# Kernel tuning notes

Hardware: AMD Instinct MI355X
Metric: run time of the kernel (lower is better)

Reference implementation:

```python
import jax, jax.numpy as jnp
import numpy as np

N, E, F_IN, H = 50000, 800000, 500, 96

def setup_inputs() -> dict:
    key = jax.random.key(0)
    ks = jax.random.split(key, 10)
    x = jax.random.normal(ks[0], (N, F_IN), dtype=jnp.float32)
    src = jax.random.randint(ks[1], (E,), 0, N, dtype=jnp.int32)
    dst = jax.random.randint(ks[2], (E,), 0, N, dtype=jnp.int32)
    perm = jax.random.permutation(ks[3], N).astype(jnp.int32)
    W1 = jax.random.normal(ks[4], (F_IN, H), dtype=jnp.float32) / np.sqrt(F_IN)
    b1 = jnp.zeros((H,), jnp.float32)
    a1 = jnp.full((H,), 0.25, jnp.float32)  # PReLU init
    W2 = jax.random.normal(ks[5], (H, H), dtype=jnp.float32) / np.sqrt(H)
    b2 = jnp.zeros((H,), jnp.float32)
    a2 = jnp.full((H,), 0.25, jnp.float32)
    Wm = jax.random.normal(ks[6], (H, H), dtype=jnp.float32) / np.sqrt(H)
    bm = jnp.zeros((H,), jnp.float32)
    return {"x": x, "src": src, "dst": dst, "perm": perm,
            "W1": W1, "b1": b1, "a1": a1, "W2": W2, "b2": b2, "a2": a2,
            "Wm": Wm, "bm": bm}

def reference(x, src, dst, perm, W1, b1, a1, W2, b2, a2, Wm, bm):
    n = x.shape[0]
    ones = jnp.ones_like(src, dtype=x.dtype)
    deg_out = jnp.clip(jax.ops.segment_sum(ones, src, num_segments=n), 1.0)
    deg_in = jnp.clip(jax.ops.segment_sum(ones, dst, num_segments=n), 1.0)
    norm_out = (deg_out ** -0.5)[:, None]  # [N,1]
    norm_in = (deg_in ** -0.5)[:, None]

    def gconv(h, W, b, a):
        # DGL GraphConv, norm='both': D_out^-1/2 -> W -> A -> D_in^-1/2 -> +b -> PReLU
        h = (h * norm_out) @ W                                  # [N,H]
        agg = jax.ops.segment_sum(h[src], dst, num_segments=n)  # SpMM via gather/scatter
        h = agg * norm_in + b
        return jnp.where(h >= 0, h, a * h)                      # PReLU

    def encode(feat):
        h = gconv(feat, W1, b1, a1)
        return gconv(h, W2, b2, a2)

    z1 = encode(x)
    z2 = encode(x[perm])  # corrupted view: permuted node features
    z1 = z1 @ Wm + bm
    z2 = z2 @ Wm + bm
    return jnp.concatenate([z1.sum(1), z2.sum(1)], axis=0)  # [2N]
```

## Files before the change

kernel.cpp:

```cpp
#include <hip/hip_runtime.h>

#define H96 96

typedef __attribute__((ext_vector_type(8))) short bf16x8_t;
typedef __attribute__((ext_vector_type(4))) float f32x4_t;
typedef __attribute__((ext_vector_type(8))) _Float16 half8_t;

__global__ void deg_kernel(const int* __restrict__ src, const int* __restrict__ dst,
                           int* __restrict__ dout, int* __restrict__ din, int E) {
    int e = blockIdx.x * blockDim.x + threadIdx.x;
    if (e < E) {
        atomicAdd(dout + src[e], 1);
        atomicAdd(din + dst[e], 1);
    }
}

__global__ void norm_kernel(const int* __restrict__ dO, const int* __restrict__ dI,
                            float* __restrict__ no, float* __restrict__ ni, int N) {
    int i = blockIdx.x * blockDim.x + threadIdx.x;
    if (i < N) {
        no[i] = rsqrtf(fmaxf((float)dO[i], 1.0f));
        ni[i] = rsqrtf(fmaxf((float)dI[i], 1.0f));
    }
}

__global__ void scanA_kernel(const int* __restrict__ in, int* __restrict__ pre,
                             int* __restrict__ bsums, int n) {
    __shared__ int s[256];
    int i = blockIdx.x * 256 + threadIdx.x;
    int v = (i < n) ? in[i] : 0;
    s[threadIdx.x] = v;
    __syncthreads();
    for (int off = 1; off < 256; off <<= 1) {
        int t = (threadIdx.x >= off) ? s[threadIdx.x - off] : 0;
        __syncthreads();
        s[threadIdx.x] += t;
        __syncthreads();
    }
    if (i < n) pre[i] = s[threadIdx.x] - v;
    if (threadIdx.x == 255) bsums[blockIdx.x] = s[255];
}

__global__ void scanB_kernel(int* __restrict__ bsums, int nb) {
    __shared__ int s[256];
    int v = (threadIdx.x < nb) ? bsums[threadIdx.x] : 0;
    s[threadIdx.x] = v;
    __syncthreads();
    for (int off = 1; off < 256; off <<= 1) {
        int t = (threadIdx.x >= off) ? s[threadIdx.x - off] : 0;
        __syncthreads();
        s[threadIdx.x] += t;
        __syncthreads();
    }
    if (threadIdx.x < nb) bsums[threadIdx.x] = s[threadIdx.x] - v;
}

__global__ void rowfin_kernel(const int* __restrict__ pre, const int* __restrict__ bsums,
                              int* __restrict__ row_start, int* __restrict__ cursor,
                              int N, int E) {
    int i = blockIdx.x * 256 + threadIdx.x;
    if (i < N) {
        int v = pre[i] + bsums[blockIdx.x];
        row_start[i] = v;
        cursor[i] = v;
    }
    if (i == 0) row_start[N] = E;
}

__global__ void scatter_kernel(const int* __restrict__ src, const int* __restrict__ dst,
                               const int* __restrict__ perm, const float* __restrict__ norm_out,
                               int* __restrict__ cursor, int4* __restrict__ edge4, int E) {
    int e = blockIdx.x * 256 + threadIdx.x;
    if (e < E) {
        int d = dst[e];
        int s = src[e];
        int p = atomicAdd(cursor + d, 1);
        edge4[p] = make_int4(s, perm[s], __float_as_int(norm_out[s]), 0);
    }
}

__global__ void histblk_kernel(const int* __restrict__ deg, int* __restrict__ hb,
                               int N, int nb) {
    __shared__ int h[256];
    h[threadIdx.x] = 0;
    __syncthreads();
    int i = blockIdx.x * 256 + threadIdx.x;
    if (i < N) atomicAdd(&h[min(deg[i], 255)], 1);
    __syncthreads();
    hb[threadIdx.x * nb + blockIdx.x] = h[threadIdx.x];
}

__global__ void place2_kernel(const int* __restrict__ deg, const int* __restrict__ hpre,
                              const int* __restrict__ bsums, int* __restrict__ order,
                              int N, int nb) {
    __shared__ int cur[256];
    int idx = threadIdx.x * nb + blockIdx.x;
    cur[threadIdx.x] = hpre[idx] + bsums[idx >> 8];
    __syncthreads();
    int i = blockIdx.x * 256 + threadIdx.x;
    if (i < N) {
        int b = min(deg[i], 255);
        int p = atomicAdd(&cur[b], 1);
        order[p] = i;
    }
}

__device__ __forceinline__ void f2bf2(float v, unsigned short& h, unsigned short& l) {
    unsigned int b = __float_as_uint(v);
    unsigned short hh = (unsigned short)((b + 0x7FFFu + ((b >> 16) & 1u)) >> 16);
    float fh = __uint_as_float(((unsigned int)hh) << 16);
    float r = v - fh;
    unsigned int rb = __float_as_uint(r);
    unsigned short ll = (unsigned short)((rb + 0x7FFFu + ((rb >> 16) & 1u)) >> 16);
    h = hh; l = ll;
}

__global__ void weights_prep(const float* __restrict__ W1, const float* __restrict__ W2,
                             const float* __restrict__ Wm, const float* __restrict__ bm,
                             unsigned short* __restrict__ w1h, unsigned short* __restrict__ w1l,
                             unsigned short* __restrict__ w2h, unsigned short* __restrict__ w2l,
                             float* __restrict__ wsum, float* __restrict__ bsum,
                             int F, int KP1) {
    int idx = blockIdx.x * 256 + threadIdx.x;
    int z1 = 96 * KP1, z2 = z1 + 96 * 96;
    if (idx < z1) {
        int n = idx / KP1, k = idx - n * KP1;
        float v = (k < F) ? W1[(size_t)k * 96 + n] : 0.f;
        unsigned short h, l;
        f2bf2(v, h, l);
        w1h[idx] = h; w1l[idx] = l;
    } else if (idx < z2) {
        int t = idx - z1;
        int n = t / 96, k = t - n * 96;
        float v = W2[(size_t)k * 96 + n];
        unsigned short h, l;
        f2bf2(v, h, l);
        w2h[t] = h; w2l[t] = l;
    } else if (idx < z2 + 96) {
        int c = idx - z2;
        float s = 0.f;
        for (int j = 0; j < 96; j++) s += Wm[c * 96 + j];
        wsum[c] = s;
    } else if (idx == z2 + 96) {
        float s = 0.f;
        for (int j = 0; j < 96; j++) s += bm[j];
        bsum[0] = s;
    }
}

#define GBM 64
#define GBK 32
#define ASTR2 40
__global__ __launch_bounds__(256) void gemm_mfma(const void* __restrict__ Av,
                                                 const unsigned short* __restrict__ Bth,
                                                 const unsigned short* __restrict__ Btl,
                                                 _Float16* __restrict__ C16,
                                                 int M, int K, int KP, int a_half) {
    __shared__ unsigned short As_hi[GBM * ASTR2];
    __shared__ unsigned short As_lo[GBM * ASTR2];
    __shared__ unsigned short Bs_hi[96 * ASTR2];
    __shared__ unsigned short Bs_lo[96 * ASTR2];
    int tid = threadIdx.x;
    int row0 = blockIdx.x * GBM;
    int wid = tid >> 6, lane = tid & 63;
    int q = lane >> 4, mn = lane & 15;
    f32x4_t acc[6] = {};
    int nk = (K + GBK - 1) / GBK;

    const float* A32 = (const float*)Av;
    const _Float16* A16 = (const _Float16*)Av;

    for (int t = 0; t < nk; t++) {
        int k0 = t * GBK;
        if (a_half) {
            int r = tid >> 2, kq = tid & 3;
            int gr = row0 + r, gk = k0 + kq * 8;
            uint4 raw = (gr < M) ? *(const uint4*)(A16 + (size_t)gr * K + gk)
                                 : make_uint4(0, 0, 0, 0);
            const _Float16* hp = (const _Float16*)&raw;
            unsigned short hs[8], ls[8];
#pragma unroll
            for (int c = 0; c < 8; c++) f2bf2((float)hp[c], hs[c], ls[c]);
            uint4 hv, lv;
            hv.x = hs[0] | ((unsigned)hs[1] << 16); hv.y = hs[2] | ((unsigned)hs[3] << 16);
            hv.z = hs[4] | ((unsigned)hs[5] << 16); hv.w = hs[6] | ((unsigned)hs[7] << 16);
            lv.x = ls[0] | ((unsigned)ls[1] << 16); lv.y = ls[2] | ((unsigned)ls[3] << 16);
            lv.z = ls[4] | ((unsigned)ls[5] << 16); lv.w = ls[6] | ((unsigned)ls[7] << 16);
            *(uint4*)&As_hi[r * ASTR2 + kq * 8] = hv;
            *(uint4*)&As_lo[r * ASTR2 + kq * 8] = lv;
        } else {
#pragma unroll
            for (int i = 0; i < 2; i++) {
                int idx = tid + i * 256;
                int r = idx >> 3, kq = idx & 7;
                int gr = row0 + r, gk = k0 + kq * 4;
                float4 v = make_float4(0.f, 0.f, 0.f, 0.f);
                if (gr < M) {
                    if (gk + 4 <= K) {
                        v = *(const float4*)(A32 + (size_t)gr * K + gk);
                    } else {
                        float tv[4] = {0.f, 0.f, 0.f, 0.f};
                        for (int c = 0; c < 4; c++)
                            if (gk + c < K) tv[c] = A32[(size_t)gr * K + gk + c];
                        v = make_float4(tv[0], tv[1], tv[2], tv[3]);
                    }
                }
                unsigned short h0, l0, h1, l1, h2, l2, h3, l3;
                f2bf2(v.x, h0, l0); f2bf2(v.y, h1, l1);
                f2bf2(v.z, h2, l2); f2bf2(v.w, h3, l3);
                uint2 hv = make_uint2((unsigned)h0 | ((unsigned)h1 << 16),
                                      (unsigned)h2 | ((unsigned)h3 << 16));
                uint2 lv = make_uint2((unsigned)l0 | ((unsigned)l1 << 16),
                                      (unsigned)l2 | ((unsigned)l3 << 16));
                *(uint2*)&As_hi[r * ASTR2 + kq * 4] = hv;
                *(uint2*)&As_lo[r * ASTR2 + kq * 4] = lv;
            }
        }
#pragma unroll
        for (int i = 0; i < 2; i++) {
            int idx = tid + i * 256;
            if (idx < 384) {
                int n = idx >> 2, kc = idx & 3;
                uint4 hv = *(const uint4*)(Bth + (size_t)n * KP + k0 + kc * 8);
                uint4 lv = *(const uint4*)(Btl + (size_t)n * KP + k0 + kc * 8);
                *(uint4*)&Bs_hi[n * ASTR2 + kc * 8] = hv;
                *(uint4*)&Bs_lo[n * ASTR2 + kc * 8] = lv;
            }
        }
        __syncthreads();

        int wr = wid * 16 + mn;
        bf16x8_t ah = *(const bf16x8_t*)&As_hi[wr * ASTR2 + q * 8];
        bf16x8_t al = *(const bf16x8_t*)&As_lo[wr * ASTR2 + q * 8];
#pragma unroll
        for (int ct = 0; ct < 6; ct++) {
            int n = ct * 16 + mn;
            bf16x8_t bh = *(const bf16x8_t*)&Bs_hi[n * ASTR2 + q * 8];
            bf16x8_t bl = *(const bf16x8_t*)&Bs_lo[n * ASTR2 + q * 8];
            acc[ct] = __builtin_amdgcn_mfma_f32_16x16x32_bf16(ah, bh, acc[ct], 0, 0, 0);
            acc[ct] = __builtin_amdgcn_mfma_f32_16x16x32_bf16(ah, bl, acc[ct], 0, 0, 0);
            acc[ct] = __builtin_amdgcn_mfma_f32_16x16x32_bf16(al, bh, acc[ct], 0, 0, 0);
        }
        __syncthreads();
    }

#pragma unroll
    for (int reg = 0; reg < 4; reg++) {
        int gr = row0 + wid * 16 + q * 4 + reg;
        if (gr < M) {
#pragma unroll
            for (int ct = 0; ct < 6; ct++)
                C16[(size_t)gr * H96 + ct * 16 + mn] = (_Float16)acc[ct][reg];
        }
    }
}

__device__ __forceinline__ void fmah8(float4& a, float4& b, float s, half8_t v) {
    a.x = fmaf(s, (float)v[0], a.x); a.y = fmaf(s, (float)v[1], a.y);
    a.z = fmaf(s, (float)v[2], a.z); a.w = fmaf(s, (float)v[3], a.w);
    b.x = fmaf(s, (float)v[4], b.x); b.y = fmaf(s, (float)v[5], b.y);
    b.z = fmaf(s, (float)v[6], b.z); b.w = fmaf(s, (float)v[7], b.w);
}

__device__ __forceinline__ float4 prelu4(float4 acc, float ni, float4 b, float4 a) {
    float4 h;
    h.x = fmaf(acc.x, ni, b.x); h.x = (h.x >= 0.f) ? h.x : a.x * h.x;
    h.y = fmaf(acc.y, ni, b.y); h.y = (h.y >= 0.f) ? h.y : a.y * h.y;
    h.z = fmaf(acc.z, ni, b.z); h.z = (h.z >= 0.f) ? h.z : a.z * h.z;
    h.w = fmaf(acc.w, ni, b.w); h.w = (h.w >= 0.f) ? h.w : a.w * h.w;
    return h;
}

__global__ __launch_bounds__(384) void spmm1_dual(
        const half8_t* __restrict__ yh, const int* __restrict__ row_start,
        const int4* __restrict__ edge4, const int* __restrict__ order,
        const float* __restrict__ norm_out, const float* __restrict__ norm_in,
        const float* __restrict__ b1, const float* __restrict__ a1,
        half8_t* __restrict__ h1, half8_t* __restrict__ h2, int N) {
    int g = blockIdx.x * 32 + threadIdx.y;
    if (g >= N) return;
    int d = order[g];
    int tx = threadIdx.x;
    int beg = row_start[d], end = row_start[d + 1];
    const half8_t* yt = yh + tx;
    float4 a1a = {0,0,0,0}, a1b = {0,0,0,0}, a2a = {0,0,0,0}, a2b = {0,0,0,0};
    int j = beg;
    for (; j + 8 <= end; j += 8) {
        int4 e[8];
#pragma unroll
        for (int q = 0; q < 8; q++) e[q] = edge4[j + q];
        half8_t u[8], w[8];
#pragma unroll
        for (int q = 0; q < 8; q++) u[q] = yt[(size_t)e[q].x * 12];
#pragma unroll
        for (int q = 0; q < 8; q++) w[q] = yt[(size_t)e[q].y * 12];
#pragma unroll
        for (int q = 0; q < 8; q++) {
            float n = __int_as_float(e[q].z);
            fmah8(a1a, a1b, n, u[q]);
            fmah8(a2a, a2b, n, w[q]);
        }
    }
    for (; j < end; j++) {
        int4 e = edge4[j];
        float n = __int_as_float(e.z);
        fmah8(a1a, a1b, n, yt[(size_t)e.x * 12]);
        fmah8(a2a, a2b, n, yt[(size_t)e.y * 12]);
    }
    float ni = norm_in[d], no = norm_out[d];
    float4 bb0 = ((const float4*)b1)[tx * 2], bb1 = ((const float4*)b1)[tx * 2 + 1];
    float4 aa0 = ((const float4*)a1)[tx * 2], aa1 = ((const float4*)a1)[tx * 2 + 1];
    float4 r1a = prelu4(a1a, ni, bb0, aa0), r1b = prelu4(a1b, ni, bb1, aa1);
    float4 r2a = prelu4(a2a, ni, bb0, aa0), r2b = prelu4(a2b, ni, bb1, aa1);
    half8_t o1, o2;
    o1[0] = (_Float16)(r1a.x * no); o1[1] = (_Float16)(r1a.y * no);
    o1[2] = (_Float16)(r1a.z * no); o1[3] = (_Float16)(r1a.w * no);
    o1[4] = (_Float16)(r1b.x * no); o1[5] = (_Float16)(r1b.y * no);
    o1[6] = (_Float16)(r1b.z * no); o1[7] = (_Float16)(r1b.w * no);
    o2[0] = (_Float16)(r2a.x * no); o2[1] = (_Float16)(r2a.y * no);
    o2[2] = (_Float16)(r2a.z * no); o2[3] = (_Float16)(r2a.w * no);
    o2[4] = (_Float16)(r2b.x * no); o2[5] = (_Float16)(r2b.y * no);
    o2[6] = (_Float16)(r2b.z * no); o2[7] = (_Float16)(r2b.w * no);
    h1[(size_t)d * 12 + tx] = o1;
    h2[(size_t)d * 12 + tx] = o2;
}

__global__ __launch_bounds__(384) void spmm2_dual(
        const half8_t* __restrict__ th,
        const int* __restrict__ row_start, const int4* __restrict__ edge4,
        const int* __restrict__ order, const float* __restrict__ norm_in,
        const float* __restrict__ b2, const float* __restrict__ a2,
        const float* __restrict__ wsum, const float* __restrict__ bsum,
        float* __restrict__ outp, int N) {
    int g = blockIdx.x * 32 + threadIdx.y;
    int tx = threadIdx.x;
    int ty = threadIdx.y;
    bool valid = (g < N);
    int d = valid ? order[g] : 0;
    int beg = 0, end = 0;
    if (valid) { beg = row_start[d]; end = row_start[d + 1]; }
    const half8_t* t1 = th + tx;
    const half8_t* t2 = th + (size_t)N * 12 + tx;
    float4 a1a = {0,0,0,0}, a1b = {0,0,0,0}, a2a = {0,0,0,0}, a2b = {0,0,0,0};
    int j = beg;
    for (; j + 8 <= end; j += 8) {
        int s[8];
#pragma unroll
        for (int q = 0; q < 8; q++) s[q] = edge4[j + q].x;
        half8_t u[8], w[8];
#pragma unroll
        for (int q = 0; q < 8; q++) u[q] = t1[(size_t)s[q] * 12];
#pragma unroll
        for (int q = 0; q < 8; q++) w[q] = t2[(size_t)s[q] * 12];
#pragma unroll
        for (int q = 0; q < 8; q++) {
            fmah8(a1a, a1b, 1.f, u[q]);
            fmah8(a2a, a2b, 1.f, w[q]);
        }
    }
    for (; j < end; j++) {
        int s = edge4[j].x;
        fmah8(a1a, a1b, 1.f, t1[(size_t)s * 12]);
        fmah8(a2a, a2b, 1.f, t2[(size_t)s * 12]);
    }
    float ni = valid ? norm_in[d] : 0.f;
    float4 bb0 = ((const float4*)b2)[tx * 2], bb1 = ((const float4*)b2)[tx * 2 + 1];
    float4 aa0 = ((const float4*)a2)[tx * 2], aa1 = ((const float4*)a2)[tx * 2 + 1];
    float4 wv0 = ((const float4*)wsum)[tx * 2], wv1 = ((const float4*)wsum)[tx * 2 + 1];
    float4 r1a = prelu4(a1a, ni, bb0, aa0), r1b = prelu4(a1b, ni, bb1, aa1);
    float4 r2a = prelu4(a2a, ni, bb0, aa0), r2b = prelu4(a2b, ni, bb1, aa1);
    float p1 = r1a.x * wv0.x + r1a.y * wv0.y + r1a.z * wv0.z + r1a.w * wv0.w
             + r1b.x * wv1.x + r1b.y * wv1.y + r1b.z * wv1.z + r1b.w * wv1.w;
    float p2 = r2a.x * wv0.x + r2a.y * wv0.y + r2a.z * wv0.z + r2a.w * wv0.w
             + r2b.x * wv1.x + r2b.y * wv1.y + r2b.z * wv1.z + r2b.w * wv1.w;
    __shared__ float red1[32][12];
    __shared__ float red2[32][12];
    red1[ty][tx] = p1;
    red2[ty][tx] = p2;
    __syncthreads();
    if (tx == 0 && valid) {
        float s1 = 0.f, s2 = 0.f;
#pragma unroll
        for (int k = 0; k < 12; k++) { s1 += red1[ty][k]; s2 += red2[ty][k]; }
        outp[d] = s1 + bsum[0];
        outp[N + d] = s2 + bsum[0];
    }
}

extern "C" void kernel_launch(void* const* d_in, const int* in_sizes, int n_in,
                              void* d_out, int out_size, void* d_ws, size_t ws_size,
                              hipStream_t stream) {
    const float* x    = (const float*)d_in[0];
    const int*   src  = (const int*)d_in[1];
    const int*   dst  = (const int*)d_in[2];
    const int*   perm = (const int*)d_in[3];
    const float* W1   = (const float*)d_in[4];
    const float* b1   = (const float*)d_in[5];
    const float* a1   = (const float*)d_in[6];
    const float* W2   = (const float*)d_in[7];
    const float* b2   = (const float*)d_in[8];
    const float* a2   = (const float*)d_in[9];
    const float* Wm   = (const float*)d_in[10];
    const float* bm   = (const float*)d_in[11];
    float* out = (float*)d_out;

    int E = in_sizes[1];
    int N = in_sizes[3];
    int F = in_sizes[0] / N;
    int KP1 = ((F + GBK - 1) / GBK) * GBK;

    size_t NP = ((size_t)N + 256) & ~(size_t)255;
    size_t EP = ((size_t)E + 255) & ~(size_t)255;
    int nb = (N + 255) / 256;
    size_t HB = ((size_t)256 * nb + 255) & ~(size_t)255;

    int* deg_out   = (int*)d_ws;
    int* deg_in    = deg_out + NP;
    int* pre       = deg_in + NP;
    int* row_start = pre + NP;
    int* cursor    = row_start + NP;
    int* order     = cursor + NP;
    int* bsums     = order + NP;
    int* hb        = bsums + 256;
    int* hpre      = hb + HB;
    int4* edge4    = (int4*)(hpre + HB);
    float* norm_out = (float*)(edge4 + EP);
    float* norm_in  = norm_out + NP;
    float* wsum     = norm_in + NP;
    float* bsum     = wsum + 128;
    unsigned short* w1th = (unsigned short*)(bsum + 128);
    unsigned short* w1tl = w1th + 49664;
    unsigned short* w2th = w1tl + 49664;
    unsigned short* w2tl = w2th + 9728;
    _Float16* yh  = (_Float16*)(w2tl + 9728);
    _Float16* h1h = yh + ((size_t)N * H96 + 256);
    _Float16* th  = h1h + ((size_t)2 * N * H96 + 256);

    hipMemsetAsync(deg_out, 0, 2 * NP * sizeof(int), stream);
    deg_kernel<<<(E + 255) / 256, 256, 0, stream>>>(src, dst, deg_out, deg_in, E);
    norm_kernel<<<(N + 255) / 256, 256, 0, stream>>>(deg_out, deg_in, norm_out, norm_in, N);

    scanA_kernel<<<nb, 256, 0, stream>>>(deg_in, pre, bsums, N);
    scanB_kernel<<<1, 256, 0, stream>>>(bsums, nb);
    rowfin_kernel<<<nb, 256, 0, stream>>>(pre, bsums, row_start, cursor, N, E);
    scatter_kernel<<<(E + 255) / 256, 256, 0, stream>>>(src, dst, perm, norm_out, cursor,
                                                        edge4, E);

    histblk_kernel<<<nb, 256, 0, stream>>>(deg_in, hb, N, nb);
    int n2 = 256 * nb;
    int nb2 = (n2 + 255) / 256;
    scanA_kernel<<<nb2, 256, 0, stream>>>(hb, hpre, bsums, n2);
    scanB_kernel<<<1, 256, 0, stream>>>(bsums, nb2);
    place2_kernel<<<nb, 256, 0, stream>>>(deg_in, hpre, bsums, order, N, nb);

    int wtot = 96 * KP1 + 96 * 96 + 96 + 1;
    weights_prep<<<(wtot + 255) / 256, 256, 0, stream>>>(W1, W2, Wm, bm, w1th, w1tl,
                                                         w2th, w2tl, wsum, bsum, F, KP1);

    gemm_mfma<<<(N + GBM - 1) / GBM, 256, 0, stream>>>(x, w1th, w1tl, yh, N, F, KP1, 0);

    int nsb = (N + 31) / 32;
    spmm1_dual<<<nsb, dim3(12, 32), 0, stream>>>(
        (const half8_t*)yh, row_start, edge4, order, norm_out, norm_in,
        b1, a1, (half8_t*)h1h, (half8_t*)(h1h + (size_t)N * H96), N);

    gemm_mfma<<<(2 * N + GBM - 1) / GBM, 256, 0, stream>>>(h1h, w2th, w2tl, th, 2 * N, H96, H96, 1);

    spmm2_dual<<<nsb, dim3(12, 32), 0, stream>>>(
        (const half8_t*)th, row_start, edge4, order, norm_in, b2, a2,
        wsum, bsum, out, N);
}
```

Before: 445.2 us.

## Use LDS-histogram degree counting and LDS-free register-direct MFMA GEMM

Degree counting drops global atomics, memset and the separate norm kernel. Edge chunks are now histogrammed per node bucket in shared memory, and a reduce kernel sums the partial histograms and writes both norms and deg_in. Separately, the GEMM no longer stages A and B tiles through LDS with block barriers. Each lane loads its A fragment directly, splits it to bf16 hi/lo in registers, and reads B fragments from global/cache per MFMA. This removes syncs and LDS traffic but re-reads B from cache per wave and adds partial-histogram memory traffic.

```diff
diff --git a/kernel.cpp b/kernel.cpp
--- a/kernel.cpp
+++ b/kernel.cpp
@@ -1,27 +1,50 @@
 #include <hip/hip_runtime.h>
 
 #define H96 96
+#define BUCK 8192
+#define DEGC 24
 
 typedef __attribute__((ext_vector_type(8))) short bf16x8_t;
 typedef __attribute__((ext_vector_type(4))) float f32x4_t;
 typedef __attribute__((ext_vector_type(8))) _Float16 half8_t;
 
-__global__ void deg_kernel(const int* __restrict__ src, const int* __restrict__ dst,
-                           int* __restrict__ dout, int* __restrict__ din, int E) {
-    int e = blockIdx.x * blockDim.x + threadIdx.x;
-    if (e < E) {
-        atomicAdd(dout + src[e], 1);
-        atomicAdd(din + dst[e], 1);
-    }
-}
-
-__global__ void norm_kernel(const int* __restrict__ dO, const int* __restrict__ dI,
-                            float* __restrict__ no, float* __restrict__ ni, int N) {
-    int i = blockIdx.x * blockDim.x + threadIdx.x;
-    if (i < N) {
-        no[i] = rsqrtf(fmaxf((float)dO[i], 1.0f));
-        ni[i] = rsqrtf(fmaxf((float)dI[i], 1.0f));
-    }
+__global__ __launch_bounds__(256) void degpart_kernel(const int* __restrict__ src,
+                                                      const int* __restrict__ dst,
+                                                      int* __restrict__ partial,
+                                                      int N, int E, int nchunk) {
+    __shared__ int h[BUCK];
+    for (int i = threadIdx.x; i < BUCK; i += 256) h[i] = 0;
+    __syncthreads();
+    const int* arr = blockIdx.z ? dst : src;
+    int lo = blockIdx.x * BUCK;
+    int per = (E + nchunk - 1) / nchunk;
+    int e0 = blockIdx.y * per;
+    int e1 = min(e0 + per, E);
+    for (int e = e0 + threadIdx.x; e < e1; e += 256) {
+        int v = arr[e] - lo;
+        if ((unsigned)v < BUCK) atomicAdd(&h[v], 1);
+    }
+    __syncthreads();
+    size_t base = ((size_t)blockIdx.z * nchunk + blockIdx.y) * N;
+    for (int i = threadIdx.x; i < BUCK; i += 256) {
+        int node = lo + i;
+        if (node < N) partial[base + node] = h[i];
+    }
+}
+
+__global__ void degreduce_kernel(const int* __restrict__ partial, float* __restrict__ no,
+                                 float* __restrict__ ni, int* __restrict__ deg_in,
+                                 int N, int nchunk) {
+    int i = blockIdx.x * 256 + threadIdx.x;
+    if (i >= N) return;
+    int s0 = 0, s1 = 0;
+    for (int c = 0; c < nchunk; c++) {
+        s0 += partial[(size_t)c * N + i];
+        s1 += partial[((size_t)nchunk + c) * N + i];
+    }
+    no[i] = rsqrtf(fmaxf((float)s0, 1.0f));
+    ni[i] = rsqrtf(fmaxf((float)s1, 1.0f));
+    deg_in[i] = s1;
 }
 
 __global__ void scanA_kernel(const int* __restrict__ in, int* __restrict__ pre,
@@ -148,105 +171,62 @@
     }
 }
 
-#define GBM 64
-#define GBK 32
-#define ASTR2 40
 __global__ __launch_bounds__(256) void gemm_mfma(const void* __restrict__ Av,
                                                  const unsigned short* __restrict__ Bth,
                                                  const unsigned short* __restrict__ Btl,
                                                  _Float16* __restrict__ C16,
                                                  int M, int K, int KP, int a_half) {
-    __shared__ unsigned short As_hi[GBM * ASTR2];
-    __shared__ unsigned short As_lo[GBM * ASTR2];
-    __shared__ unsigned short Bs_hi[96 * ASTR2];
-    __shared__ unsigned short Bs_lo[96 * ASTR2];
-    int tid = threadIdx.x;
-    int row0 = blockIdx.x * GBM;
-    int wid = tid >> 6, lane = tid & 63;
+    int wid = threadIdx.x >> 6, lane = threadIdx.x & 63;
     int q = lane >> 4, mn = lane & 15;
-    f32x4_t acc[6] = {};
-    int nk = (K + GBK - 1) / GBK;
-
+    int rbase = blockIdx.x * 64 + wid * 16;
+    int row = rbase + mn;
+    bool rowok = (row < M);
     const float* A32 = (const float*)Av;
     const _Float16* A16 = (const _Float16*)Av;
+    f32x4_t acc[6] = {};
+    int nk = (K + 31) / 32;
 
     for (int t = 0; t < nk; t++) {
-        int k0 = t * GBK;
+        int gk = t * 32 + q * 8;
+        float av[8];
         if (a_half) {
-            int r = tid >> 2, kq = tid & 3;
-            int gr = row0 + r, gk = k0 + kq * 8;
-            uint4 raw = (gr < M) ? *(const uint4*)(A16 + (size_t)gr * K + gk)
-                                 : make_uint4(0, 0, 0, 0);
+            uint4 raw = rowok ? *(const uint4*)(A16 + (size_t)row * K + gk)
+                              : make_uint4(0, 0, 0, 0);
             const _Float16* hp = (const _Float16*)&raw;
-            unsigned short hs[8], ls[8];
-#pragma unroll
-            for (int c = 0; c < 8; c++) f2bf2((float)hp[c], hs[c], ls[c]);
-            uint4 hv, lv;
-            hv.x = hs[0] | ((unsigned)hs[1] << 16); hv.y = hs[2] | ((unsigned)hs[3] << 16);
-            hv.z = hs[4] | ((unsigned)hs[5] << 16); hv.w = hs[6] | ((unsigned)hs[7] << 16);
-            lv.x = ls[0] | ((unsigned)ls[1] << 16); lv.y = ls[2] | ((unsigned)ls[3] << 16);
-            lv.z = ls[4] | ((unsigned)ls[5] << 16); lv.w = ls[6] | ((unsigned)ls[7] << 16);
-            *(uint4*)&As_hi[r * ASTR2 + kq * 8] = hv;
-            *(uint4*)&As_lo[r * ASTR2 + kq * 8] = lv;
+#pragma unroll
+            for (int c = 0; c < 8; c++) av[c] = (float)hp[c];
+        } else if (rowok && gk + 8 <= K) {
+            float4 v0 = *(const float4*)(A32 + (size_t)row * K + gk);
+            float4 v1 = *(const float4*)(A32 + (size_t)row * K + gk + 4);
+            av[0] = v0.x; av[1] = v0.y; av[2] = v0.z; av[3] = v0.w;
+            av[4] = v1.x; av[5] = v1.y; av[6] = v1.z; av[7] = v1.w;
         } else {
 #pragma unroll
-            for (int i = 0; i < 2; i++) {
-                int idx = tid + i * 256;
-                int r = idx >> 3, kq = idx & 7;
-                int gr = row0 + r, gk = k0 + kq * 4;
-                float4 v = make_float4(0.f, 0.f, 0.f, 0.f);
-                if (gr < M) {
-                    if (gk + 4 <= K) {
-                        v = *(const float4*)(A32 + (size_t)gr * K + gk);
-                    } else {
-                        float tv[4] = {0.f, 0.f, 0.f, 0.f};
-                        for (int c = 0; c < 4; c++)
-                            if (gk + c < K) tv[c] = A32[(size_t)gr * K + gk + c];
-                        v = make_float4(tv[0], tv[1], tv[2], tv[3]);
-                    }
-                }
-                unsigned short h0, l0, h1, l1, h2, l2, h3, l3;
-                f2bf2(v.x, h0, l0); f2bf2(v.y, h1, l1);
-                f2bf2(v.z, h2, l2); f2bf2(v.w, h3, l3);
-                uint2 hv = make_uint2((unsigned)h0 | ((unsigned)h1 << 16),
-                                      (unsigned)h2 | ((unsigned)h3 << 16));
-                uint2 lv = make_uint2((unsigned)l0 | ((unsigned)l1 << 16),
-                                      (unsigned)l2 | ((unsigned)l3 << 16));
-                *(uint2*)&As_hi[r * ASTR2 + kq * 4] = hv;
-                *(uint2*)&As_lo[r * ASTR2 + kq * 4] = lv;
-            }
-        }
-#pragma unroll
-        for (int i = 0; i < 2; i++) {
-            int idx = tid + i * 256;
-            if (idx < 384) {
-                int n = idx >> 2, kc = idx & 3;
-                uint4 hv = *(const uint4*)(Bth + (size_t)n * KP + k0 + kc * 8);
-                uint4 lv = *(const uint4*)(Btl + (size_t)n * KP + k0 + kc * 8);
-                *(uint4*)&Bs_hi[n * ASTR2 + kc * 8] = hv;
-                *(uint4*)&Bs_lo[n * ASTR2 + kc * 8] = lv;
-            }
-        }
-        __syncthreads();
-
-        int wr = wid * 16 + mn;
-        bf16x8_t ah = *(const bf16x8_t*)&As_hi[wr * ASTR2 + q * 8];
-        bf16x8_t al = *(const bf16x8_t*)&As_lo[wr * ASTR2 + q * 8];
+            for (int c = 0; c < 8; c++)
+                av[c] = (rowok && gk + c < K) ? A32[(size_t)row * K + gk + c] : 0.f;
+        }
+        bf16x8_t ah, al;
+#pragma unroll
+        for (int c = 0; c < 8; c++) {
+            unsigned short h, l;
+            f2bf2(av[c], h, l);
+            ah[c] = (short)h;
+            al[c] = (short)l;
+        }
 #pragma unroll
         for (int ct = 0; ct < 6; ct++) {
-            int n = ct * 16 + mn;
-            bf16x8_t bh = *(const bf16x8_t*)&Bs_hi[n * ASTR2 + q * 8];
-            bf16x8_t bl = *(const bf16x8_t*)&Bs_lo[n * ASTR2 + q * 8];
+            size_t boff = (size_t)(ct * 16 + mn) * KP + gk;
+            bf16x8_t bh = *(const bf16x8_t*)(Bth + boff);
+            bf16x8_t bl = *(const bf16x8_t*)(Btl + boff);
             acc[ct] = __builtin_amdgcn_mfma_f32_16x16x32_bf16(ah, bh, acc[ct], 0, 0, 0);
             acc[ct] = __builtin_amdgcn_mfma_f32_16x16x32_bf16(ah, bl, acc[ct], 0, 0, 0);
             acc[ct] = __builtin_amdgcn_mfma_f32_16x16x32_bf16(al, bh, acc[ct], 0, 0, 0);
         }
-        __syncthreads();
     }
 
 #pragma unroll
     for (int reg = 0; reg < 4; reg++) {
-        int gr = row0 + wid * 16 + q * 4 + reg;
+        int gr = rbase + q * 4 + reg;
         if (gr < M) {
 #pragma unroll
             for (int ct = 0; ct < 6; ct++)
@@ -407,15 +387,14 @@
     int E = in_sizes[1];
     int N = in_sizes[3];
     int F = in_sizes[0] / N;
-    int KP1 = ((F + GBK - 1) / GBK) * GBK;
+    int KP1 = ((F + 31) / 32) * 32;
 
     size_t NP = ((size_t)N + 256) & ~(size_t)255;
     size_t EP = ((size_t)E + 255) & ~(size_t)255;
     int nb = (N + 255) / 256;
     size_t HB = ((size_t)256 * nb + 255) & ~(size_t)255;
 
-    int* deg_out   = (int*)d_ws;
-    int* deg_in    = deg_out + NP;
+    int* deg_in    = (int*)d_ws;
     int* pre       = deg_in + NP;
     int* row_start = pre + NP;
     int* cursor    = row_start + NP;
@@ -423,7 +402,8 @@
     int* bsums     = order + NP;
     int* hb        = bsums + 256;
     int* hpre      = hb + HB;
-    int4* edge4    = (int4*)(hpre + HB);
+    int* partial   = hpre + HB;
+    int4* edge4    = (int4*)(partial + (size_t)2 * DEGC * NP);
     float* norm_out = (float*)(edge4 + EP);
     float* norm_in  = norm_out + NP;
     float* wsum     = norm_in + NP;
@@ -436,9 +416,9 @@
     _Float16* h1h = yh + ((size_t)N * H96 + 256);
     _Float16* th  = h1h + ((size_t)2 * N * H96 + 256);
 
-    hipMemsetAsync(deg_out, 0, 2 * NP * sizeof(int), stream);
-    deg_kernel<<<(E + 255) / 256, 256, 0, stream>>>(src, dst, deg_out, deg_in, E);
-    norm_kernel<<<(N + 255) / 256, 256, 0, stream>>>(deg_out, deg_in, norm_out, norm_in, N);
+    int nbuck = (N + BUCK - 1) / BUCK;
+    degpart_kernel<<<dim3(nbuck, DEGC, 2), 256, 0, stream>>>(src, dst, partial, N, E, DEGC);
+    degreduce_kernel<<<nb, 256, 0, stream>>>(partial, norm_out, norm_in, deg_in, N, DEGC);
 
     scanA_kernel<<<nb, 256, 0, stream>>>(deg_in, pre, bsums, N);
     scanB_kernel<<<1, 256, 0, stream>>>(bsums, nb);
@@ -457,14 +437,14 @@
     weights_prep<<<(wtot + 255) / 256, 256, 0, stream>>>(W1, W2, Wm, bm, w1th, w1tl,
                                                          w2th, w2tl, wsum, bsum, F, KP1);
 
-    gemm_mfma<<<(N + GBM - 1) / GBM, 256, 0, stream>>>(x, w1th, w1tl, yh, N, F, KP1, 0);
+    gemm_mfma<<<(N + 63) / 64, 256, 0, stream>>>(x, w1th, w1tl, yh, N, F, KP1, 0);
 
     int nsb = (N + 31) / 32;
     spmm1_dual<<<nsb, dim3(12, 32), 0, stream>>>(
         (const half8_t*)yh, row_start, edge4, order, norm_out, norm_in,
         b1, a1, (half8_t*)h1h, (half8_t*)(h1h + (size_t)N * H96), N);
 
-    gemm_mfma<<<(2 * N + GBM - 1) / GBM, 256, 0, stream>>>(h1h, w2th, w2tl, th, 2 * N, H96, H96, 1);
+    gemm_mfma<<<(2 * N + 63) / 64, 256, 0, stream>>>(h1h, w2th, w2tl, th, 2 * N, H96, H96, 1);
 
     spmm2_dual<<<nsb, dim3(12, 32), 0, stream>>>(
         (const half8_t*)th, row_start, edge4, order, norm_in, b2, a2,
```

Result: slower. 501.6 us (+12.7%).
